# Kernel tuning notes

Measured on AMD Instinct MI355X. Metric: run time of the kernel, lower is better.

The kernel has to match this reference:

```python
import jax, jax.numpy as jnp
import numpy as np

N_NODES = 50000
N_REL = 4
N_EDGES = 800000
IN_DIM = 128
HID = 128
N_CLASSES = 16


def setup_inputs() -> dict:
    key = jax.random.key(0)
    ks = jax.random.split(key, 12)
    feat = jax.random.normal(ks[0], (N_NODES, IN_DIM), dtype=jnp.float32)
    src = jax.random.randint(ks[1], (N_REL, N_EDGES), 0, N_NODES, dtype=jnp.int32)
    dst = jax.random.randint(ks[2], (N_REL, N_EDGES), 0, N_NODES, dtype=jnp.int32)
    s = 0.05
    W1 = jax.random.normal(ks[3], (N_REL, IN_DIM, HID), dtype=jnp.float32) * s
    b1 = jax.random.normal(ks[4], (N_REL, HID), dtype=jnp.float32) * s
    W2 = jax.random.normal(ks[5], (N_REL, HID, HID), dtype=jnp.float32) * s
    b2 = jax.random.normal(ks[6], (N_REL, HID), dtype=jnp.float32) * s
    W3 = jax.random.normal(ks[7], (N_REL, HID, HID), dtype=jnp.float32) * s
    b3 = jax.random.normal(ks[8], (N_REL, HID), dtype=jnp.float32) * s
    Wlin = jax.random.normal(ks[9], (HID, N_CLASSES), dtype=jnp.float32) * s
    blin = jax.random.normal(ks[10], (N_CLASSES,), dtype=jnp.float32) * s
    return {"feat": feat, "src": src, "dst": dst, "W1": W1, "b1": b1,
            "W2": W2, "b2": b2, "W3": W3, "b3": b3, "Wlin": Wlin, "blin": blin}


def _graph_conv(x, s, d, W, b, n_nodes):
    """DGL GraphConv with norm='both': D_dst^-1/2 * A * D_src^-1/2 * x, then @W + b."""
    ones = jnp.ones(s.shape[0], dtype=x.dtype)
    deg_out = jnp.maximum(jax.ops.segment_sum(ones, s, num_segments=n_nodes), 1.0)
    deg_in = jnp.maximum(jax.ops.segment_sum(ones, d, num_segments=n_nodes), 1.0)
    xs = x * (deg_out ** -0.5)[:, None]          # [N, F]
    agg = jax.ops.segment_sum(xs[s], d, num_segments=n_nodes)  # gather+scatter [N, F]
    agg = agg * (deg_in ** -0.5)[:, None]
    return agg @ W + b


def _hetero_layer(x, src, dst, W, b, n_nodes):
    # HeteroGraphConv aggregate='sum' over relations (loop over small fixed R)
    out = _graph_conv(x, src[0], dst[0], W[0], b[0], n_nodes)
    for r in range(1, src.shape[0]):
        out = out + _graph_conv(x, src[r], dst[r], W[r], b[r], n_nodes)
    return out


def _l2_normalize(x, eps=1e-12):
    # torch F.normalize: x / max(||x||_2, eps), per row
    nrm = jnp.sqrt(jnp.sum(x * x, axis=1, keepdims=True))
    return x / jnp.maximum(nrm, eps)


def reference(feat, src, dst, W1, b1, W2, b2, W3, b3, Wlin, blin):
    n = feat.shape[0]
    h = _hetero_layer(feat, src, dst, W1, b1, n)
    h = jax.nn.leaky_relu(_l2_normalize(h), negative_slope=0.01)
    h = _hetero_layer(h, src, dst, W2, b2, n)
    h = jax.nn.leaky_relu(_l2_normalize(h), negative_slope=0.01)
    h = _hetero_layer(h, src, dst, W3, b3, n)
    # update_all(copy_u, sum) across all relations (unnormalized scatter-sum)
    pooled = jax.ops.segment_sum(h[src[0]], dst[0], num_segments=n)
    for r in range(1, src.shape[0]):
        pooled = pooled + jax.ops.segment_sum(h[src[r]], dst[r], num_segments=n)
    hg = jnp.mean(pooled, axis=0, keepdims=True)  # dgl.mean_nodes -> [1, HID]
    return jax.nn.sigmoid(hg @ Wlin + blin)       # [1, n_classes]
```

## Files before the change

### kernel.cpp

```cpp
#include <hip/hip_runtime.h>
#include <hip/hip_bf16.h>

constexpr int N_NODES = 50000;
constexpr int N_REL   = 4;
constexpr int N_EDGES = 800000;
constexpr int DIM     = 128;
constexpr int N_CLS   = 16;

constexpr int CHUNK  = 256;
constexpr int NCHUNK = (N_NODES + CHUNK - 1) / CHUNK;
constexpr int NPART  = N_REL * NCHUNK;

constexpr int NCBR  = (N_NODES + 255) / 256;
constexpr int NCB   = N_REL * NCBR;
constexpr int TILE  = 8000;
constexpr int TPR   = N_EDGES / TILE;
constexpr int MAXB  = 6144;

constexpr int RNG    = 12544;
constexpr int NRANGE = 4;
constexpr int DTILE  = 80000;
constexpr int DNT    = N_EDGES / DTILE;

constexpr int NPB = 8;
constexpr int CAP = 512;

constexpr int N_PAD = 50048;

constexpr float YSCALE = 32.0f;

typedef __attribute__((ext_vector_type(8))) short short8;
typedef __attribute__((ext_vector_type(4))) float float4v;
typedef __attribute__((ext_vector_type(2))) float floatx2;

__device__ __forceinline__ unsigned int f2bf_bits(float f) {
  unsigned int u = __float_as_uint(f);
  return (u + 0x7fffu + ((u >> 16) & 1u)) >> 16;
}
__device__ __forceinline__ unsigned int pack2bf(float a, float b) {
  return f2bf_bits(a) | (f2bf_bits(b) << 16);
}
__device__ __forceinline__ float bf_lo(unsigned int u) { return __uint_as_float(u << 16); }
__device__ __forceinline__ float bf_hi(unsigned int u) { return __uint_as_float(u & 0xffff0000u); }

__device__ __forceinline__ int LCOL(int p) { return (p & 7) * 16 + (p >> 3); }

__global__ __launch_bounds__(256) void degree_hist(
    const int* __restrict__ src, const int* __restrict__ dst,
    int* __restrict__ cnt_out, int* __restrict__ cnt_in) {
  int b = blockIdx.x;
  int t     = b % DNT;    b /= DNT;
  int range = b % NRANGE; b /= NRANGE;
  int r     = b % N_REL;  b /= N_REL;
  int which = b;
  const int* arr = (which ? dst : src) + (size_t)r * N_EDGES + (size_t)t * DTILE;
  int* cnt = (which ? cnt_in : cnt_out) + r * N_NODES;
  int tid = threadIdx.x;
  __shared__ int h[RNG];
  for (int i = tid; i < RNG; i += 256) h[i] = 0;
  __syncthreads();
  int lo = range * RNG;
  int hi = lo + RNG;
  const int4* a4 = (const int4*)arr;
  for (int i = tid; i < DTILE / 4; i += 256) {
    int4 v = a4[i];
    if (v.x >= lo && v.x < hi) atomicAdd(&h[v.x - lo], 1);
    if (v.y >= lo && v.y < hi) atomicAdd(&h[v.y - lo], 1);
    if (v.z >= lo && v.z < hi) atomicAdd(&h[v.z - lo], 1);
    if (v.w >= lo && v.w < hi) atomicAdd(&h[v.w - lo], 1);
  }
  __syncthreads();
  for (int i = tid; i < RNG; i += 256) {
    int n = lo + i;
    int c = h[i];
    if (n < N_NODES && c) atomicAdd(&cnt[n], c);
  }
}

__global__ __launch_bounds__(256) void scan_partial(
    const int* __restrict__ cnt_in, int* __restrict__ partial) {
  int b = blockIdx.x;
  int r = b / NCHUNK, c = b % NCHUNK;
  int i = c * CHUNK + threadIdx.x;
  int v = (i < N_NODES) ? cnt_in[r * N_NODES + i] : 0;
#pragma unroll
  for (int off = 1; off < 64; off <<= 1) v += __shfl_xor(v, off, 64);
  __shared__ int ws[4];
  if ((threadIdx.x & 63) == 0) ws[threadIdx.x >> 6] = v;
  __syncthreads();
  if (threadIdx.x == 0) partial[b] = ws[0] + ws[1] + ws[2] + ws[3];
}

__global__ __launch_bounds__(1024) void scan_offsets(
    const int* __restrict__ partial, int* __restrict__ chunk_off,
    int* __restrict__ row_ptr) {
  __shared__ int lds[1024];
  __shared__ int sexcl[1024];
  __shared__ int stotal;
  int tid = threadIdx.x;
  int v = (tid < NPART) ? partial[tid] : 0;
  lds[tid] = v;
  __syncthreads();
  for (int off = 1; off < 1024; off <<= 1) {
    int t = (tid >= off) ? lds[tid - off] : 0;
    __syncthreads();
    lds[tid] += t;
    __syncthreads();
  }
  int excl = lds[tid] - v;
  sexcl[tid] = excl;
  if (tid == NPART - 1) stotal = excl + v;
  if (tid < NPART) chunk_off[tid] = excl;
  __syncthreads();
  if (tid < N_REL) {
    int base = sexcl[tid * NCHUNK];
    int next = (tid < N_REL - 1) ? sexcl[(tid + 1) * NCHUNK] : stotal;
    row_ptr[tid * (N_NODES + 1) + N_NODES] = next - base;
  }
}

__global__ __launch_bounds__(256) void scan_expand(
    const int* __restrict__ cnt_in, const int* __restrict__ chunk_off,
    int* __restrict__ row_ptr, int* __restrict__ cbcur,
    const int* __restrict__ cnt_out, float* __restrict__ soutF,
    float* __restrict__ sinF, float* __restrict__ wout) {
  int b = blockIdx.x;
  int r = b / NCHUNK, c = b % NCHUNK;
  int tid = threadIdx.x;
  int i = c * CHUNK + tid;
  int v = (i < N_NODES) ? cnt_in[r * N_NODES + i] : 0;
  __shared__ int lds[CHUNK];
  lds[tid] = v;
  __syncthreads();
  for (int off = 1; off < CHUNK; off <<= 1) {
    int t = (tid >= off) ? lds[tid - off] : 0;
    __syncthreads();
    lds[tid] += t;
    __syncthreads();
  }
  int excl = lds[tid] - v;
  int base = chunk_off[b] - chunk_off[r * NCHUNK];
  if (i < N_NODES) {
    row_ptr[r * (N_NODES + 1) + i] = base + excl;
    int co = cnt_out[r * N_NODES + i];
    soutF[r * N_NODES + i] = YSCALE / sqrtf((float)max(co, 1));
    sinF [r * N_NODES + i] = (1.0f / YSCALE) / sqrtf((float)max(v, 1));
    if (r == 0) {
      wout[i] = (float)(co + cnt_out[N_NODES + i] +
                        cnt_out[2 * N_NODES + i] + cnt_out[3 * N_NODES + i]);
    }
  }
  if (tid == 0) cbcur[r * NCBR + c] = base;
}

__global__ __launch_bounds__(256) void pass1_bin(
    const int* __restrict__ src, const int* __restrict__ dst,
    int* __restrict__ cbcur, unsigned int* __restrict__ binned) {
  int b = blockIdx.x;
  int r = b / TPR, t = b % TPR;
  const int* sp = src + (size_t)r * N_EDGES + t * TILE;
  const int* dp = dst + (size_t)r * N_EDGES + t * TILE;
  unsigned int* outp = binned + (size_t)r * N_EDGES;
  int tid = threadIdx.x;
  __shared__ int hist[NCBR];
  __shared__ int scanb[256];
  __shared__ int gbase[NCBR];
  __shared__ int lcur[NCBR];
  for (int i = tid; i < NCBR; i += 256) hist[i] = 0;
  __syncthreads();
  for (int i = tid; i < TILE; i += 256) atomicAdd(&hist[dp[i] >> 8], 1);
  __syncthreads();
  int v = (tid < NCBR) ? hist[tid] : 0;
  scanb[tid] = v;
  __syncthreads();
  for (int off = 1; off < 256; off <<= 1) {
    int tv = (tid >= off) ? scanb[tid - off] : 0;
    __syncthreads();
    scanb[tid] += tv;
    __syncthreads();
  }
  if (tid < NCBR) {
    int excl = scanb[tid] - v;
    gbase[tid] = atomicAdd(&cbcur[r * NCBR + tid], v) - excl;
    lcur[tid] = excl;
  }
  __syncthreads();
  for (int i = tid; i < TILE; i += 256) {
    int d = dp[i];
    int s = sp[i];
    int cb = d >> 8;
    int lp = atomicAdd(&lcur[cb], 1);
    outp[gbase[cb] + lp] = ((unsigned)s << 8) | (unsigned)(d & 255);
  }
}

__global__ __launch_bounds__(256) void pass2_sort(
    const unsigned int* __restrict__ binned, const int* __restrict__ row_ptr,
    unsigned short* __restrict__ csr) {
  int b = blockIdx.x;
  int r = b / NCBR, c = b % NCBR;
  int node0 = c * 256;
  int node1 = min(node0 + 256, N_NODES);
  int start = row_ptr[r * (N_NODES + 1) + node0];
  int endv  = row_ptr[r * (N_NODES + 1) + node1];
  int count = endv - start;
  const unsigned int* bp = binned + (size_t)r * N_EDGES + start;
  unsigned short* outg = csr + (size_t)r * N_EDGES + start;
  int tid = threadIdx.x;
  __shared__ int hist[4096];
  __shared__ int scanb[256];
  __shared__ unsigned short outb[MAXB];
  for (int i = tid; i < 4096; i += 256) hist[i] = 0;
  __syncthreads();
  for (int i = tid; i < count; i += 256) {
    unsigned int p = bp[i];
    unsigned int key = ((p & 255u) << 4) | ((p >> 8) >> 12);
    atomicAdd(&hist[key], 1);
  }
  __syncthreads();
  int t16 = tid * 16;
  int a[16];
  int tsum = 0;
#pragma unroll
  for (int j = 0; j < 16; ++j) { a[j] = hist[t16 + j]; tsum += a[j]; }
  scanb[tid] = tsum;
  __syncthreads();
  for (int off = 1; off < 256; off <<= 1) {
    int tv = (tid >= off) ? scanb[tid - off] : 0;
    __syncthreads();
    scanb[tid] += tv;
    __syncthreads();
  }
  int run = scanb[tid] - tsum;
#pragma unroll
  for (int j = 0; j < 16; ++j) { hist[t16 + j] = run; run += a[j]; }
  __syncthreads();
  if (count <= MAXB) {
    for (int i = tid; i < count; i += 256) {
      unsigned int p = bp[i];
      unsigned int s = p >> 8;
      unsigned int key = ((p & 255u) << 4) | (s >> 12);
      int pos = atomicAdd(&hist[key], 1);
      outb[pos] = (unsigned short)s;
    }
    __syncthreads();
    for (int i = tid; i < count; i += 256) outg[i] = outb[i];
  } else {
    for (int i = tid; i < count; i += 256) {
      unsigned int p = bp[i];
      unsigned int s = p >> 8;
      unsigned int key = ((p & 255u) << 4) | (s >> 12);
      int pos = atomicAdd(&hist[key], 1);
      outg[pos] = (unsigned short)s;
    }
  }
}

__global__ __launch_bounds__(256) void prep_w3(
    const float* __restrict__ W1, const float* __restrict__ b1,
    const float* __restrict__ W2, const float* __restrict__ b2,
    const float* __restrict__ W3, const float* __restrict__ b3,
    unsigned short* __restrict__ Wt1, float* __restrict__ bs1,
    unsigned short* __restrict__ Wt2, float* __restrict__ bs2,
    unsigned short* __restrict__ Wt3, float* __restrict__ bs3) {
  int set = blockIdx.x >> 8;
  int i   = (blockIdx.x & 255) * 256 + threadIdx.x;
  const float* W = (set == 0) ? W1 : (set == 1) ? W2 : W3;
  const float* b = (set == 0) ? b1 : (set == 1) ? b2 : b3;
  unsigned short* Wt = (set == 0) ? Wt1 : (set == 1) ? Wt2 : Wt3;
  float* bsum = (set == 0) ? bs1 : (set == 1) ? bs2 : bs3;
  int permk = (set != 0);
  if (i < N_REL * DIM * DIM) {
    int col = i >> 7, p = i & 127;
    int k = permk ? LCOL(p) : p;
    int rrel = col >> 7, n = col & 127;
    Wt[i] = (unsigned short)f2bf_bits(W[rrel * DIM * DIM + k * DIM + n]);
  }
  if (i < DIM) {
    int Lp = LCOL(i);
    bsum[i] = b[Lp] + b[DIM + Lp] + b[2 * DIM + Lp] + b[3 * DIM + Lp];
  }
}

__global__ __launch_bounds__(256) void zero_pad(unsigned char* __restrict__ Yb) {
  constexpr int PER = (N_PAD - N_NODES) * DIM / 16;
  int tid = blockIdx.x * 256 + threadIdx.x;
  int r = tid / PER, k = tid % PER;
  if (r < N_REL) {
    uint4* p = (uint4*)(Yb + (size_t)r * N_PAD * DIM + (size_t)N_NODES * DIM);
    p[k] = make_uint4(0u, 0u, 0u, 0u);
  }
}

template <int AF32>
__global__ __launch_bounds__(256) void gemm_y(
    const void* __restrict__ Xv, const unsigned short* __restrict__ Wt,
    const float* __restrict__ soutF, unsigned char* __restrict__ Yb) {
  int tid = threadIdx.x;
  int w   = tid >> 6;
  int l   = tid & 63;
  int l15 = l & 15, lq = l >> 4;
  int rowbase = blockIdx.x * 64;

  const unsigned short* X = (const unsigned short*)Xv;
  const float*          Xf = (const float*)Xv;

  float4v acc[4][8] = {};
  const unsigned short* Wq = Wt + (size_t)(w * DIM) * DIM;

#pragma unroll
  for (int ks = 0; ks < 4; ++ks) {
    int k0 = ks * 32 + lq * 8;
    short8 bfr[8];
#pragma unroll
    for (int c = 0; c < 8; ++c)
      bfr[c] = *(const short8*)(Wq + (size_t)(c * 16 + l15) * DIM + k0);
#pragma unroll
    for (int i = 0; i < 4; ++i) {
      int rr = rowbase + i * 16 + l15;
      short8 afr;
      if (rr < N_NODES) {
        if (AF32) {
          const float* xp = Xf + (size_t)rr * DIM + k0;
          float4 f0 = *(const float4*)xp;
          float4 f1 = *(const float4*)(xp + 4);
          afr[0] = (short)f2bf_bits(f0.x);
          afr[1] = (short)f2bf_bits(f0.y);
          afr[2] = (short)f2bf_bits(f0.z);
          afr[3] = (short)f2bf_bits(f0.w);
          afr[4] = (short)f2bf_bits(f1.x);
          afr[5] = (short)f2bf_bits(f1.y);
          afr[6] = (short)f2bf_bits(f1.z);
          afr[7] = (short)f2bf_bits(f1.w);
        } else {
          afr = *(const short8*)(X + (size_t)rr * DIM + k0);
        }
      } else {
        afr = (short8)(short)0;
      }
#pragma unroll
      for (int c = 0; c < 8; ++c)
        acc[i][c] = __builtin_amdgcn_mfma_f32_16x16x32_bf16(afr, bfr[c],
                                                            acc[i][c], 0, 0, 0);
    }
  }

  const float* so = soutF + (size_t)w * N_NODES;
  unsigned char* Yq = Yb + (size_t)w * N_PAD * DIM;
#pragma unroll
  for (int i = 0; i < 4; ++i) {
#pragma unroll
    for (int rr = 0; rr < 4; ++rr) {
      int grow = rowbase + i * 16 + lq * 4 + rr;
      if (grow < N_NODES) {
        float sc = so[grow];
        float v0 = acc[i][0][rr] * sc, v1 = acc[i][1][rr] * sc;
        float v2 = acc[i][2][rr] * sc, v3 = acc[i][3][rr] * sc;
        float v4 = acc[i][4][rr] * sc, v5 = acc[i][5][rr] * sc;
        float v6 = acc[i][6][rr] * sc, v7 = acc[i][7][rr] * sc;
        int t0 = __builtin_amdgcn_cvt_pk_fp8_f32(v0, v1, 0, false);
        t0 = __builtin_amdgcn_cvt_pk_fp8_f32(v2, v3, t0, true);
        int t1 = __builtin_amdgcn_cvt_pk_fp8_f32(v4, v5, 0, false);
        t1 = __builtin_amdgcn_cvt_pk_fp8_f32(v6, v7, t1, true);
        uint2 o;
        o.x = (unsigned)t0;
        o.y = (unsigned)t1;
        *(uint2*)(Yq + (size_t)grow * DIM + l15 * 8) = o;
      }
    }
  }
}

template <int MODE>
__global__ __launch_bounds__(256) void gather_y(
    const unsigned char* __restrict__ Yb, const unsigned short* __restrict__ csr,
    const int* __restrict__ row_ptr, const float* __restrict__ sinF,
    const float* __restrict__ bsum, void* __restrict__ out) {
  int d0   = blockIdx.x * NPB;
  int r    = threadIdx.x >> 6;
  int lane = threadIdx.x & 63;
  int g    = lane >> 4;
  int l16  = lane & 15;
  const unsigned short* cs = csr + (size_t)r * N_EDGES;
  const unsigned char*  Yq = Yb + (size_t)r * N_PAD * DIM;

  int rp = row_ptr[r * (N_NODES + 1) + d0 + min(lane, NPB)];
  int beg0 = __shfl(rp, 0, 64);
  int cnt  = __shfl(rp, NPB, 64) - beg0;

  __shared__ unsigned short scsr[N_REL][CAP];
  __shared__ __align__(16) unsigned int ubuf[N_REL][NPB][66];

  int ccap = min(cnt, CAP);
  for (int i = lane; i < ccap; i += 64) scsr[r][i] = cs[beg0 + i];

  auto body = [&](auto CS) {
#pragma unroll 1
    for (int n = 0; n < NPB; n += 2) {
      int bA = __shfl(rp, n, 64),  eA = __shfl(rp, n + 1, 64);
      int bB = eA,                 eB = __shfl(rp, n + 2, 64);
      floatx2 aA[4], aB[4];
#pragma unroll
      for (int j = 0; j < 4; ++j) {
        aA[j] = (floatx2){0.f, 0.f};
        aB[j] = (floatx2){0.f, 0.f};
      }
      int pA = bA, pB = bB;
      while (pA < eA || pB < eB) {
        bool doA = pA < eA, doB = pB < eB;
        uint2 xA[4], xB[4];
        if (doA) {
#pragma unroll
          for (int u = 0; u < 4; ++u) {
            int e = pA + u * 4 + g;
            int se = (e < eA) ? (int)CS(e) : N_NODES;
            xA[u] = *(const uint2*)(Yq + (size_t)se * DIM + l16 * 8);
          }
        }
        if (doB) {
#pragma unroll
          for (int u = 0; u < 4; ++u) {
            int e = pB + u * 4 + g;
            int se = (e < eB) ? (int)CS(e) : N_NODES;
            xB[u] = *(const uint2*)(Yq + (size_t)se * DIM + l16 * 8);
          }
        }
        if (doA) {
#pragma unroll
          for (int u = 0; u < 4; ++u) {
            aA[0] += __builtin_amdgcn_cvt_pk_f32_fp8((int)xA[u].x, false);
            aA[1] += __builtin_amdgcn_cvt_pk_f32_fp8((int)xA[u].x, true);
            aA[2] += __builtin_amdgcn_cvt_pk_f32_fp8((int)xA[u].y, false);
            aA[3] += __builtin_amdgcn_cvt_pk_f32_fp8((int)xA[u].y, true);
          }
          pA += 16;
        }
        if (doB) {
#pragma unroll
          for (int u = 0; u < 4; ++u) {
            aB[0] += __builtin_amdgcn_cvt_pk_f32_fp8((int)xB[u].x, false);
            aB[1] += __builtin_amdgcn_cvt_pk_f32_fp8((int)xB[u].x, true);
            aB[2] += __builtin_amdgcn_cvt_pk_f32_fp8((int)xB[u].y, false);
            aB[3] += __builtin_amdgcn_cvt_pk_f32_fp8((int)xB[u].y, true);
          }
          pB += 16;
        }
      }
#pragma unroll
      for (int j = 0; j < 4; ++j) {
        aA[j].x += __shfl_xor(aA[j].x, 16, 64);
        aA[j].y += __shfl_xor(aA[j].y, 16, 64);
        aA[j].x += __shfl_xor(aA[j].x, 32, 64);
        aA[j].y += __shfl_xor(aA[j].y, 32, 64);
        aB[j].x += __shfl_xor(aB[j].x, 16, 64);
        aB[j].y += __shfl_xor(aB[j].y, 16, 64);
        aB[j].x += __shfl_xor(aB[j].x, 32, 64);
        aB[j].y += __shfl_xor(aB[j].y, 32, 64);
      }
      if (g < 2) {
        uint2 wA, wB;
        if (g == 0) {
          wA.x = pack2bf(aA[0].x, aA[0].y); wA.y = pack2bf(aA[1].x, aA[1].y);
          wB.x = pack2bf(aB[0].x, aB[0].y); wB.y = pack2bf(aB[1].x, aB[1].y);
        } else {
          wA.x = pack2bf(aA[2].x, aA[2].y); wA.y = pack2bf(aA[3].x, aA[3].y);
          wB.x = pack2bf(aB[2].x, aB[2].y); wB.y = pack2bf(aB[3].x, aB[3].y);
        }
        *(uint2*)&ubuf[r][n][l16 * 4 + g * 2]     = wA;
        *(uint2*)&ubuf[r][n + 1][l16 * 4 + g * 2] = wB;
      }
    }
  };
  if (cnt <= CAP)
    body([&](int e) { return scsr[r][e - beg0]; });
  else
    body([&](int e) { return cs[e]; });
  __syncthreads();

  int nn = threadIdx.x >> 5;
  int ln = threadIdx.x & 31;
  int d  = d0 + nn;
  float s0 = sinF[d];
  float s1 = sinF[N_NODES + d];
  float s2 = sinF[2 * N_NODES + d];
  float s3 = sinF[3 * N_NODES + d];
  uint2 u0 = *(const uint2*)&ubuf[0][nn][ln * 2];
  uint2 u1 = *(const uint2*)&ubuf[1][nn][ln * 2];
  uint2 u2 = *(const uint2*)&ubuf[2][nn][ln * 2];
  uint2 u3 = *(const uint2*)&ubuf[3][nn][ln * 2];
  float4 bs = *(const float4*)&bsum[ln * 4];
  float v0 = s0 * bf_lo(u0.x) + s1 * bf_lo(u1.x) + s2 * bf_lo(u2.x) +
             s3 * bf_lo(u3.x) + bs.x;
  float v1 = s0 * bf_hi(u0.x) + s1 * bf_hi(u1.x) + s2 * bf_hi(u2.x) +
             s3 * bf_hi(u3.x) + bs.y;
  float v2 = s0 * bf_lo(u0.y) + s1 * bf_lo(u1.y) + s2 * bf_lo(u2.y) +
             s3 * bf_lo(u3.y) + bs.z;
  float v3 = s0 * bf_hi(u0.y) + s1 * bf_hi(u1.y) + s2 * bf_hi(u2.y) +
             s3 * bf_hi(u3.y) + bs.w;
  if (MODE == 1) {
    float ss = v0 * v0 + v1 * v1 + v2 * v2 + v3 * v3;
    ss += __shfl_xor(ss, 1, 32);
    ss += __shfl_xor(ss, 2, 32);
    ss += __shfl_xor(ss, 4, 32);
    ss += __shfl_xor(ss, 8, 32);
    ss += __shfl_xor(ss, 16, 32);
    float sc = 1.0f / fmaxf(sqrtf(ss), 1e-12f);
    v0 *= sc; v1 *= sc; v2 *= sc; v3 *= sc;
    v0 = v0 > 0.f ? v0 : 0.01f * v0;
    v1 = v1 > 0.f ? v1 : 0.01f * v1;
    v2 = v2 > 0.f ? v2 : 0.01f * v2;
    v3 = v3 > 0.f ? v3 : 0.01f * v3;
    uint2 o;
    o.x = pack2bf(v0, v1);
    o.y = pack2bf(v2, v3);
    *(uint2*)((unsigned short*)out + (size_t)d * DIM + ln * 4) = o;
  } else {
    float4 o = make_float4(v0, v1, v2, v3);
    *(float4*)((float*)out + (size_t)d * DIM + ln * 4) = o;
  }
}

__global__ __launch_bounds__(256) void pool_kernel(
    const float* __restrict__ h, const float* __restrict__ wout,
    float* __restrict__ hg) {
  int gw   = blockIdx.x * 4 + (threadIdx.x >> 6);
  int lane = threadIdx.x & 63;
  int nw   = gridDim.x * 4;
  float ax = 0.0f, ay = 0.0f;
  for (int v = gw; v < N_NODES; v += nw) {
    float w = wout[v];
    float2 hv = *(const float2*)(h + (size_t)v * DIM + lane * 2);
    ax = fmaf(w, hv.x, ax);
    ay = fmaf(w, hv.y, ay);
  }
  atomicAdd(&hg[lane * 2],     ax);
  atomicAdd(&hg[lane * 2 + 1], ay);
}

__global__ void head_kernel(const float* __restrict__ hg,
                            const float* __restrict__ Wlin,
                            const float* __restrict__ blin,
                            float* __restrict__ out) {
  int j = threadIdx.x;
  if (j < N_CLS) {
    float s = blin[j];
    const float invN = 1.0f / (float)N_NODES;
#pragma unroll 16
    for (int k = 0; k < DIM; ++k) {
      int Lk = (k & 7) * 16 + (k >> 3);
      s = fmaf(hg[k] * invN, Wlin[Lk * N_CLS + j], s);
    }
    out[j] = 1.0f / (1.0f + expf(-s));
  }
}

__global__ void fail_kernel(float* out) {
  int i = threadIdx.x;
  if (i < N_CLS) out[i] = 1e30f;
}

extern "C" void kernel_launch(void* const* d_in, const int* in_sizes, int n_in,
                              void* d_out, int out_size, void* d_ws, size_t ws_size,
                              hipStream_t stream) {
  const float* feat = (const float*)d_in[0];
  const int*   src  = (const int*)  d_in[1];
  const int*   dst  = (const int*)  d_in[2];
  const float* W1   = (const float*)d_in[3];
  const float* b1   = (const float*)d_in[4];
  const float* W2   = (const float*)d_in[5];
  const float* b2   = (const float*)d_in[6];
  const float* W3   = (const float*)d_in[7];
  const float* b3   = (const float*)d_in[8];
  const float* Wlin = (const float*)d_in[9];
  const float* blin = (const float*)d_in[10];
  float* out = (float*)d_out;

  char* base = (char*)d_ws;
  size_t off = 0;
  auto alloc = [&](size_t bytes) -> void* {
    void* q = base + off;
    off = (off + bytes + 255) & ~(size_t)255;
    return q;
  };
  int*   cnt_out  = (int*)  alloc((size_t)N_REL * N_NODES * 4);
  int*   cnt_in   = (int*)  alloc((size_t)N_REL * N_NODES * 4);
  int*   row_ptr  = (int*)  alloc((size_t)N_REL * (N_NODES + 1) * 4);
  float* soutF    = (float*)alloc((size_t)N_REL * N_NODES * 4);
  float* sinF     = (float*)alloc((size_t)N_REL * N_NODES * 4);
  float* wout     = (float*)alloc((size_t)N_NODES * 4);
  float* hg       = (float*)alloc((size_t)DIM * 4);
  int*   partial  = (int*)  alloc((size_t)NPART * 4);
  int*   chunkoff = (int*)  alloc((size_t)NPART * 4);
  int*   cbcur    = (int*)  alloc((size_t)NCB * 4);
  unsigned int*   binned = (unsigned int*)  alloc((size_t)N_REL * N_EDGES * 4);
  unsigned short* csr    = (unsigned short*)alloc((size_t)N_REL * N_EDGES * 2);
  unsigned char*  Yb     = (unsigned char*) alloc((size_t)N_REL * N_PAD * DIM);
  unsigned short* X1     = (unsigned short*)alloc((size_t)N_NODES * DIM * 2);
  unsigned short* X2     = (unsigned short*)alloc((size_t)N_NODES * DIM * 2);
  float* H3       = (float*)alloc((size_t)N_NODES * DIM * 4);
  unsigned short* Wt1 = (unsigned short*)alloc((size_t)N_REL * DIM * DIM * 2);
  unsigned short* Wt2 = (unsigned short*)alloc((size_t)N_REL * DIM * DIM * 2);
  unsigned short* Wt3 = (unsigned short*)alloc((size_t)N_REL * DIM * DIM * 2);
  float* bs1 = (float*)alloc(DIM * 4);
  float* bs2 = (float*)alloc(DIM * 4);
  float* bs3 = (float*)alloc(DIM * 4);

  if (off > ws_size) {
    fail_kernel<<<1, 64, 0, stream>>>(out);
    return;
  }

  hipMemsetAsync(cnt_out, 0, (size_t)2 * N_REL * N_NODES * 4, stream);
  hipMemsetAsync(hg, 0, DIM * 4, stream);

  degree_hist  <<<2 * N_REL * NRANGE * DNT, 256, 0, stream>>>(src, dst, cnt_out, cnt_in);
  scan_partial <<<NPART, 256, 0, stream>>>(cnt_in, partial);
  scan_offsets <<<1, 1024, 0, stream>>>(partial, chunkoff, row_ptr);
  scan_expand  <<<NPART, 256, 0, stream>>>(cnt_in, chunkoff, row_ptr, cbcur,
                                           cnt_out, soutF, sinF, wout);
  pass1_bin    <<<N_REL * TPR, 256, 0, stream>>>(src, dst, cbcur, binned);
  pass2_sort   <<<NCB, 256, 0, stream>>>(binned, row_ptr, csr);

  prep_w3<<<3 * 256, 256, 0, stream>>>(W1, b1, W2, b2, W3, b3,
                                       Wt1, bs1, Wt2, bs2, Wt3, bs3);
  zero_pad<<<6, 256, 0, stream>>>(Yb);

  int gemm_blocks = N_PAD / 64;
  int gath_blocks = (N_NODES + NPB - 1) / NPB;

  gemm_y<1>  <<<gemm_blocks, 256, 0, stream>>>(feat, Wt1, soutF, Yb);
  gather_y<1><<<gath_blocks, 256, 0, stream>>>(Yb, csr, row_ptr, sinF, bs1, X1);
  gemm_y<0>  <<<gemm_blocks, 256, 0, stream>>>(X1, Wt2, soutF, Yb);
  gather_y<1><<<gath_blocks, 256, 0, stream>>>(Yb, csr, row_ptr, sinF, bs2, X2);
  gemm_y<0>  <<<gemm_blocks, 256, 0, stream>>>(X2, Wt3, soutF, Yb);
  gather_y<0><<<gath_blocks, 256, 0, stream>>>(Yb, csr, row_ptr, sinF, bs3, H3);

  pool_kernel<<<256, 256, 0, stream>>>(H3, wout, hg);
  head_kernel<<<1, 64, 0, stream>>>(hg, Wlin, blin, out);
}
```

Before: 488.6 us.

## Replace two-pass binned CSR sort with single atomic scatter kernel

The two-kernel CSR build is removed: a coarse bin pass by destination block and a per-block local counting sort keyed by destination and source high bits. In its place, one kernel reads src/dst as int4 and places each edge by a global atomicAdd on a per-node cursor initialised from row_ptr. This drops one launch, the 12.8 MB intermediate binned buffer and its round trip. In exchange it issues millions of global returning atomics with some contention. It also loses the within-row ordering by source, which makes float summation order nondeterministic and may reduce gather locality.

```diff
diff --git a/kernel.cpp b/kernel.cpp
--- a/kernel.cpp
+++ b/kernel.cpp
@@ -10,12 +10,6 @@
 constexpr int CHUNK  = 256;
 constexpr int NCHUNK = (N_NODES + CHUNK - 1) / CHUNK;
 constexpr int NPART  = N_REL * NCHUNK;
-
-constexpr int NCBR  = (N_NODES + 255) / 256;
-constexpr int NCB   = N_REL * NCBR;
-constexpr int TILE  = 8000;
-constexpr int TPR   = N_EDGES / TILE;
-constexpr int MAXB  = 6144;
 
 constexpr int RNG    = 12544;
 constexpr int NRANGE = 4;
@@ -121,7 +115,7 @@
 
 __global__ __launch_bounds__(256) void scan_expand(
     const int* __restrict__ cnt_in, const int* __restrict__ chunk_off,
-    int* __restrict__ row_ptr, int* __restrict__ cbcur,
+    int* __restrict__ row_ptr, int* __restrict__ cur,
     const int* __restrict__ cnt_out, float* __restrict__ soutF,
     float* __restrict__ sinF, float* __restrict__ wout) {
   int b = blockIdx.x;
@@ -141,7 +135,9 @@
   int excl = lds[tid] - v;
   int base = chunk_off[b] - chunk_off[r * NCHUNK];
   if (i < N_NODES) {
-    row_ptr[r * (N_NODES + 1) + i] = base + excl;
+    int start = base + excl;
+    row_ptr[r * (N_NODES + 1) + i] = start;
+    cur[r * N_NODES + i] = start;
     int co = cnt_out[r * N_NODES + i];
     soutF[r * N_NODES + i] = YSCALE / sqrtf((float)max(co, 1));
     sinF [r * N_NODES + i] = (1.0f / YSCALE) / sqrtf((float)max(v, 1));
@@ -150,110 +146,24 @@
                         cnt_out[2 * N_NODES + i] + cnt_out[3 * N_NODES + i]);
     }
   }
-  if (tid == 0) cbcur[r * NCBR + c] = base;
-}
-
-__global__ __launch_bounds__(256) void pass1_bin(
+}
+
+__global__ __launch_bounds__(256) void scatter_csr(
     const int* __restrict__ src, const int* __restrict__ dst,
-    int* __restrict__ cbcur, unsigned int* __restrict__ binned) {
-  int b = blockIdx.x;
-  int r = b / TPR, t = b % TPR;
-  const int* sp = src + (size_t)r * N_EDGES + t * TILE;
-  const int* dp = dst + (size_t)r * N_EDGES + t * TILE;
-  unsigned int* outp = binned + (size_t)r * N_EDGES;
-  int tid = threadIdx.x;
-  __shared__ int hist[NCBR];
-  __shared__ int scanb[256];
-  __shared__ int gbase[NCBR];
-  __shared__ int lcur[NCBR];
-  for (int i = tid; i < NCBR; i += 256) hist[i] = 0;
-  __syncthreads();
-  for (int i = tid; i < TILE; i += 256) atomicAdd(&hist[dp[i] >> 8], 1);
-  __syncthreads();
-  int v = (tid < NCBR) ? hist[tid] : 0;
-  scanb[tid] = v;
-  __syncthreads();
-  for (int off = 1; off < 256; off <<= 1) {
-    int tv = (tid >= off) ? scanb[tid - off] : 0;
-    __syncthreads();
-    scanb[tid] += tv;
-    __syncthreads();
-  }
-  if (tid < NCBR) {
-    int excl = scanb[tid] - v;
-    gbase[tid] = atomicAdd(&cbcur[r * NCBR + tid], v) - excl;
-    lcur[tid] = excl;
-  }
-  __syncthreads();
-  for (int i = tid; i < TILE; i += 256) {
-    int d = dp[i];
-    int s = sp[i];
-    int cb = d >> 8;
-    int lp = atomicAdd(&lcur[cb], 1);
-    outp[gbase[cb] + lp] = ((unsigned)s << 8) | (unsigned)(d & 255);
-  }
-}
-
-__global__ __launch_bounds__(256) void pass2_sort(
-    const unsigned int* __restrict__ binned, const int* __restrict__ row_ptr,
-    unsigned short* __restrict__ csr) {
-  int b = blockIdx.x;
-  int r = b / NCBR, c = b % NCBR;
-  int node0 = c * 256;
-  int node1 = min(node0 + 256, N_NODES);
-  int start = row_ptr[r * (N_NODES + 1) + node0];
-  int endv  = row_ptr[r * (N_NODES + 1) + node1];
-  int count = endv - start;
-  const unsigned int* bp = binned + (size_t)r * N_EDGES + start;
-  unsigned short* outg = csr + (size_t)r * N_EDGES + start;
-  int tid = threadIdx.x;
-  __shared__ int hist[4096];
-  __shared__ int scanb[256];
-  __shared__ unsigned short outb[MAXB];
-  for (int i = tid; i < 4096; i += 256) hist[i] = 0;
-  __syncthreads();
-  for (int i = tid; i < count; i += 256) {
-    unsigned int p = bp[i];
-    unsigned int key = ((p & 255u) << 4) | ((p >> 8) >> 12);
-    atomicAdd(&hist[key], 1);
-  }
-  __syncthreads();
-  int t16 = tid * 16;
-  int a[16];
-  int tsum = 0;
-#pragma unroll
-  for (int j = 0; j < 16; ++j) { a[j] = hist[t16 + j]; tsum += a[j]; }
-  scanb[tid] = tsum;
-  __syncthreads();
-  for (int off = 1; off < 256; off <<= 1) {
-    int tv = (tid >= off) ? scanb[tid - off] : 0;
-    __syncthreads();
-    scanb[tid] += tv;
-    __syncthreads();
-  }
-  int run = scanb[tid] - tsum;
-#pragma unroll
-  for (int j = 0; j < 16; ++j) { hist[t16 + j] = run; run += a[j]; }
-  __syncthreads();
-  if (count <= MAXB) {
-    for (int i = tid; i < count; i += 256) {
-      unsigned int p = bp[i];
-      unsigned int s = p >> 8;
-      unsigned int key = ((p & 255u) << 4) | (s >> 12);
-      int pos = atomicAdd(&hist[key], 1);
-      outb[pos] = (unsigned short)s;
-    }
-    __syncthreads();
-    for (int i = tid; i < count; i += 256) outg[i] = outb[i];
-  } else {
-    for (int i = tid; i < count; i += 256) {
-      unsigned int p = bp[i];
-      unsigned int s = p >> 8;
-      unsigned int key = ((p & 255u) << 4) | (s >> 12);
-      int pos = atomicAdd(&hist[key], 1);
-      outg[pos] = (unsigned short)s;
-    }
-  }
+    int* __restrict__ cur, unsigned short* __restrict__ csr) {
+  constexpr int E4 = N_EDGES / 4;
+  int idx = blockIdx.x * 256 + threadIdx.x;
+  if (idx >= N_REL * E4) return;
+  int r  = idx / E4;
+  int e4 = idx - r * E4;
+  int4 s4 = ((const int4*)(src + (size_t)r * N_EDGES))[e4];
+  int4 d4 = ((const int4*)(dst + (size_t)r * N_EDGES))[e4];
+  int* cr = cur + r * N_NODES;
+  unsigned short* co = csr + (size_t)r * N_EDGES;
+  int p0 = atomicAdd(&cr[d4.x], 1); co[p0] = (unsigned short)s4.x;
+  int p1 = atomicAdd(&cr[d4.y], 1); co[p1] = (unsigned short)s4.y;
+  int p2 = atomicAdd(&cr[d4.z], 1); co[p2] = (unsigned short)s4.z;
+  int p3 = atomicAdd(&cr[d4.w], 1); co[p3] = (unsigned short)s4.w;
 }
 
 __global__ __launch_bounds__(256) void prep_w3(
@@ -591,8 +501,7 @@
   float* hg       = (float*)alloc((size_t)DIM * 4);
   int*   partial  = (int*)  alloc((size_t)NPART * 4);
   int*   chunkoff = (int*)  alloc((size_t)NPART * 4);
-  int*   cbcur    = (int*)  alloc((size_t)NCB * 4);
-  unsigned int*   binned = (unsigned int*)  alloc((size_t)N_REL * N_EDGES * 4);
+  int*   cur      = (int*)  alloc((size_t)N_REL * N_NODES * 4);
   unsigned short* csr    = (unsigned short*)alloc((size_t)N_REL * N_EDGES * 2);
   unsigned char*  Yb     = (unsigned char*) alloc((size_t)N_REL * N_PAD * DIM);
   unsigned short* X1     = (unsigned short*)alloc((size_t)N_NODES * DIM * 2);
@@ -616,10 +525,10 @@
   degree_hist  <<<2 * N_REL * NRANGE * DNT, 256, 0, stream>>>(src, dst, cnt_out, cnt_in);
   scan_partial <<<NPART, 256, 0, stream>>>(cnt_in, partial);
   scan_offsets <<<1, 1024, 0, stream>>>(partial, chunkoff, row_ptr);
-  scan_expand  <<<NPART, 256, 0, stream>>>(cnt_in, chunkoff, row_ptr, cbcur,
+  scan_expand  <<<NPART, 256, 0, stream>>>(cnt_in, chunkoff, row_ptr, cur,
                                            cnt_out, soutF, sinF, wout);
-  pass1_bin    <<<N_REL * TPR, 256, 0, stream>>>(src, dst, cbcur, binned);
-  pass2_sort   <<<NCB, 256, 0, stream>>>(binned, row_ptr, csr);
+  scatter_csr  <<<(N_REL * N_EDGES / 4 + 255) / 256, 256, 0, stream>>>(
+      src, dst, cur, csr);
 
   prep_w3<<<3 * 256, 256, 0, stream>>>(W1, b1, W2, b2, W3, b3,
                                        Wt1, bs1, Wt2, bs2, Wt3, bs3);
```

Measured after the change: 650.6 us. +33.1%, slower.
